# Optimization experiments

Measured on AMD Instinct MI355X. Metric: run time of the kernel, lower is better.

## Reference

```python
import jax, jax.numpy as jnp
import numpy as np

B, S, D, H = 2, 2048, 1024, 16
HD = D // H  # head_dim = 64


def setup_inputs() -> dict:
    key = jax.random.key(0)
    ks = jax.random.split(key, 7)
    scale = 0.02
    return {
        "q": jax.random.normal(ks[0], (B, S, D), dtype=jnp.float32),
        "k": jax.random.normal(ks[1], (B, S, D), dtype=jnp.float32),
        "v": jax.random.normal(ks[2], (B, S, D), dtype=jnp.float32),
        "Wq": jax.random.normal(ks[3], (D, D), dtype=jnp.float32) * scale,
        "Wk": jax.random.normal(ks[4], (D, D), dtype=jnp.float32) * scale,
        "Wv": jax.random.normal(ks[5], (D, D), dtype=jnp.float32) * scale,
        "Wo": jax.random.normal(ks[6], (D, D), dtype=jnp.float32) * scale,
    }


def reference(q, k, v, Wq, Wk, Wv, Wo):
    # bias-free linear projections (torch Linear: y = x @ W.T)
    qh = (q @ Wq.T).reshape(B, S, H, HD).transpose(0, 2, 1, 3)  # b h t d
    kh = (k @ Wk.T).reshape(B, S, H, HD).transpose(0, 2, 1, 3)
    vh = (v @ Wv.T).reshape(B, S, H, HD).transpose(0, 2, 1, 3)

    scores = jnp.einsum("bhqd,bhkd->bhqk", qh, kh) / jnp.sqrt(jnp.float32(HD))
    # max_subtract: NOTE faithful to source - max taken BEFORE causal masking
    scores = scores - jnp.max(scores, axis=-1, keepdims=True)
    # causal mask (strict upper triangle -> -inf)
    causal_mask = jnp.triu(jnp.ones((S, S), dtype=bool), k=1)
    scores = jnp.where(causal_mask, -jnp.inf, scores)
    num = jnp.exp(scores)
    den = jnp.sum(num, axis=-1, keepdims=True) + 1.0  # quiet softmax (+1 denominator)
    attn = num / den

    out = jnp.einsum("bhqk,bhkd->bhqd", attn, vh)
    out = out.transpose(0, 2, 1, 3).reshape(B, S, D)  # b t (h d)
    return out @ Wo.T
```

## Files before the change

### kernel.cpp

```cpp
#include <hip/hip_runtime.h>
#include <hip/hip_bf16.h>

#define B_  2
#define S_  2048
#define D_  1024
#define H_  16
#define HD_ 64

typedef __attribute__((ext_vector_type(4))) short s16x4;
typedef __attribute__((ext_vector_type(8))) short s16x8;
typedef __attribute__((ext_vector_type(4))) float f32x4;
typedef __attribute__((ext_vector_type(8))) __bf16 bf16x8;

__device__ __forceinline__ unsigned short f2bf(float x) {
  union { float f; unsigned int u; } un; un.f = x;
  unsigned int r = un.u + 0x7fffu + ((un.u >> 16) & 1u);
  return (unsigned short)(r >> 16);
}

__device__ __forceinline__ f32x4 fz4() { f32x4 z = {0.f, 0.f, 0.f, 0.f}; return z; }

__device__ __forceinline__ f32x4 mfma32(s16x8 a, s16x8 b, f32x4 c) {
  return __builtin_amdgcn_mfma_f32_16x16x32_bf16(
      __builtin_bit_cast(bf16x8, a), __builtin_bit_cast(bf16x8, b), c, 0, 0, 0);
}

__device__ __forceinline__ void gload16(void* lds_base, const void* gsrc) {
  __builtin_amdgcn_global_load_lds(
      (const __attribute__((address_space(1))) unsigned int*)gsrc,
      (__attribute__((address_space(3))) unsigned int*)lds_base, 16, 0, 0);
}

__global__ __launch_bounds__(256) void cvt_all(const float4* __restrict__ q,
                                               const float4* __restrict__ k,
                                               const float4* __restrict__ v,
                                               const float4* __restrict__ wq,
                                               const float4* __restrict__ wk,
                                               const float4* __restrict__ wv,
                                               const float4* __restrict__ wo,
                                               uint2* __restrict__ oq, uint2* __restrict__ ok,
                                               uint2* __restrict__ ov, uint2* __restrict__ owq,
                                               uint2* __restrict__ owk, uint2* __restrict__ owv,
                                               uint2* __restrict__ owo) {
  int i = blockIdx.x * 256 + threadIdx.x;
  int st = gridDim.x * 256;
  for (; i < 4194304; i += st) {
    const float4* s; uint2* d; int off;
    if (i < 3145728) {
      int t = i >> 20; off = i & 1048575;
      s = (t == 0) ? q : (t == 1 ? k : v);
      d = (t == 0) ? oq : (t == 1 ? ok : ov);
    } else {
      int j = i - 3145728;
      int t = j >> 18; off = j & 262143;
      s = (t == 0) ? wq : (t == 1 ? wk : (t == 2 ? wv : wo));
      d = (t == 0) ? owq : (t == 1 ? owk : (t == 2 ? owv : owo));
    }
    float4 x = s[off];
    uint2 o;
    o.x = (unsigned)f2bf(x.x) | ((unsigned)f2bf(x.y) << 16);
    o.y = (unsigned)f2bf(x.z) | ((unsigned)f2bf(x.w) << 16);
    d[off] = o;
  }
}

template<int BM, int MODE, int NG>
__global__ __launch_bounds__(256) void gemm_bt(
    const unsigned short* __restrict__ A0, const unsigned short* __restrict__ A1,
    const unsigned short* __restrict__ A2,
    const unsigned short* __restrict__ W0, const unsigned short* __restrict__ W1,
    const unsigned short* __restrict__ W2,
    unsigned short* __restrict__ ob0, unsigned short* __restrict__ ob1,
    unsigned short* __restrict__ ob2, float* __restrict__ of) {
  __shared__ unsigned short As[2][BM * 32];
  __shared__ unsigned short Bs[2][128 * 32];
  const int tid  = threadIdx.x;
  const int lane = tid & 63;
  const int w    = tid >> 6;
  const int l15  = lane & 15, g = lane >> 4;

  int m0, n0;
  const unsigned short *A, *W;
  unsigned short* obf;
  float scale = 1.0f;
  if (NG == 3) {
    int swz = ((int)blockIdx.x & 7) * 96 + ((int)blockIdx.x >> 3);
    int p  = swz >> 5;
    int gi = p >> 3;
    n0 = (p & 7) * 128;
    m0 = (swz & 31) * 128;
    A   = gi == 0 ? A0 : (gi == 1 ? A1 : A2);
    W   = gi == 0 ? W0 : (gi == 1 ? W1 : W2);
    obf = gi == 0 ? ob0 : (gi == 1 ? ob1 : ob2);
    scale = (gi == 0) ? 0.125f : 1.0f;
  } else {
    int swz = ((int)blockIdx.x & 7) * 64 + ((int)blockIdx.x >> 3);
    m0 = (swz & 63) * BM;
    n0 = (swz >> 6) * 128;
    A = A0; W = W0; obf = ob0;
  }

  constexpr int MI  = (BM == 128) ? 4 : 2;
  const int wr = (w >> 1) * (MI * 16);
  const int wc = (w & 1) * 64;

  f32x4 acc[MI][4];
  #pragma unroll
  for (int i = 0; i < MI; i++)
    #pragma unroll
    for (int j = 0; j < 4; j++) acc[i][j] = fz4();

  const int srow = w * 16 + (lane >> 2);
  const int scol = ((lane & 3) ^ ((lane >> 2) & 3)) * 8;

  #define STAGE(buf, k0)                                                          \
    {                                                                             \
      _Pragma("unroll")                                                           \
      for (int i = 0; i < BM / 64; i++)                                           \
        gload16(&As[buf][(i * 64 + w * 16) * 32],                                 \
                &A[(size_t)(m0 + i * 64 + srow) * D_ + (k0) + scol]);             \
      _Pragma("unroll")                                                           \
      for (int i = 0; i < 2; i++)                                                 \
        gload16(&Bs[buf][(i * 64 + w * 16) * 32],                                 \
                &W[(size_t)(n0 + i * 64 + srow) * D_ + (k0) + scol]);             \
    }

  STAGE(0, 0);
  __syncthreads();
  int buf = 0;
  for (int t = 0; t < 32; ++t) {
    if (t < 31) STAGE(buf ^ 1, (t + 1) * 32);
    s16x8 af[MI], bfr[4];
    #pragma unroll
    for (int mi = 0; mi < MI; mi++)
      af[mi] = *(const s16x8*)&As[buf][(wr + mi * 16 + l15) * 32 + ((g ^ (l15 & 3)) * 8)];
    #pragma unroll
    for (int ni = 0; ni < 4; ni++)
      bfr[ni] = *(const s16x8*)&Bs[buf][(wc + ni * 16 + l15) * 32 + ((g ^ (l15 & 3)) * 8)];
    __builtin_amdgcn_s_setprio(1);
    #pragma unroll
    for (int mi = 0; mi < MI; mi++)
      #pragma unroll
      for (int ni = 0; ni < 4; ni++)
        acc[mi][ni] = mfma32(af[mi], bfr[ni], acc[mi][ni]);
    __builtin_amdgcn_s_setprio(0);
    __syncthreads();
    buf ^= 1;
  }
  #undef STAGE

  #pragma unroll
  for (int mi = 0; mi < MI; mi++)
    #pragma unroll
    for (int ni = 0; ni < 4; ni++)
      #pragma unroll
      for (int j = 0; j < 4; j++) {
        int r = m0 + wr + mi * 16 + 4 * g + j;
        int c = n0 + wc + ni * 16 + l15;
        float v = acc[mi][ni][j] * scale;
        if (MODE == 0) {
          int b = r >> 11, s = r & (S_ - 1), h = c >> 6, hd = c & 63;
          obf[(((size_t)(b * H_ + h)) * S_ + s) * HD_ + hd] = f2bf(v);
        } else {
          of[(size_t)r * D_ + c] = v;
        }
      }
}

__global__ __launch_bounds__(256) void attn_kernel(const unsigned short* __restrict__ Qh,
                                                   const unsigned short* __restrict__ Kh,
                                                   const unsigned short* __restrict__ Vh,
                                                   unsigned short* __restrict__ AO) {
  __shared__ unsigned short Ks[2][64 * 64];
  __shared__ unsigned short Vt[2][64 * 76];
  const int tid  = threadIdx.x;
  const int lane = tid & 63;
  const int w    = tid >> 6;
  const int l15  = lane & 15, g = lane >> 4;

  int swz = (blockIdx.x & 7) * 128 + (blockIdx.x >> 3);
  const int qt = swz & 31;
  const int bh = swz >> 5;
  const int q0 = qt * 64;
  const unsigned short* Qb = Qh + (size_t)bh * S_ * HD_;
  const unsigned short* Kb = Kh + (size_t)bh * S_ * HD_;
  const unsigned short* Vb = Vh + (size_t)bh * S_ * HD_;

  const int qrow = q0 + w * 16 + l15;
  s16x8 qf[2];
  #pragma unroll
  for (int kk = 0; kk < 2; kk++)
    qf[kk] = *(const s16x8*)&Qb[(size_t)qrow * HD_ + kk * 32 + 8 * g];

  float m = -INFINITY, l = 0.f;
  f32x4 outa[4];
  #pragma unroll
  for (int d = 0; d < 4; d++) outa[d] = fz4();

  const int srow = w * 8 + (lane >> 3);
  const int scol = ((lane & 7) ^ ((lane >> 3) & 7)) * 8;
  const int vkey = tid & 63;

  #define STAGE_K(kblk, b)                                                        \
    {                                                                             \
      _Pragma("unroll")                                                           \
      for (int i = 0; i < 2; i++)                                                 \
        gload16(&Ks[b][(i * 256 + w * 64) * 8],                                   \
                &Kb[(size_t)((kblk) * 64 + i * 32 + srow) * HD_ + scol]);         \
    }
  #define LOAD_V(kblk, vr)                                                        \
    {                                                                             \
      _Pragma("unroll")                                                           \
      for (int r = 0; r < 2; r++)                                                 \
        vr[r] = *(const uint4*)&Vb[(size_t)((kblk) * 64 + vkey) * HD_ + (w + r * 4) * 8]; \
    }
  #define WRITE_V(b, vr)                                                          \
    {                                                                             \
      _Pragma("unroll")                                                           \
      for (int r = 0; r < 2; r++) {                                               \
        int hd0 = (w + r * 4) * 8;                                                \
        unsigned int u[4] = {vr[r].x, vr[r].y, vr[r].z, vr[r].w};                 \
        _Pragma("unroll")                                                         \
        for (int c2 = 0; c2 < 4; c2++) {                                          \
          Vt[b][(hd0 + 2 * c2    ) * 76 + vkey] = (unsigned short)(u[c2] & 0xffffu); \
          Vt[b][(hd0 + 2 * c2 + 1) * 76 + vkey] = (unsigned short)(u[c2] >> 16);  \
        }                                                                         \
      }                                                                           \
    }

  {
    STAGE_K(0, 0);
    uint4 vr0[2];
    LOAD_V(0, vr0);
    WRITE_V(0, vr0);
    __syncthreads();
  }

  for (int t = 0; t < 32; ++t) {
    const int cur = t & 1, o = cur ^ 1;
    const int k0 = t * 64;
    if (t < 31) STAGE_K(t + 1, o);
    uint4 vr[2];
    const bool vnext = (t < 31) && (t + 1 <= qt);
    if (vnext) LOAD_V(t + 1, vr);

    f32x4 sf[4];
    #pragma unroll
    for (int kt = 0; kt < 4; kt++) sf[kt] = fz4();
    __builtin_amdgcn_s_setprio(1);
    #pragma unroll
    for (int kt = 0; kt < 4; kt++)
      #pragma unroll
      for (int kk = 0; kk < 2; kk++) {
        s16x8 kf = *(const s16x8*)&Ks[cur][(kt * 16 + l15) * 64 + (((kk * 4 + g) ^ (l15 & 7)) * 8)];
        sf[kt] = mfma32(kf, qf[kk], sf[kt]);
      }
    __builtin_amdgcn_s_setprio(0);

    float bm = -INFINITY;
    #pragma unroll
    for (int kt = 0; kt < 4; kt++)
      #pragma unroll
      for (int j = 0; j < 4; j++) bm = fmaxf(bm, sf[kt][j]);
    bm = fmaxf(bm, __shfl_xor(bm, 16));
    bm = fmaxf(bm, __shfl_xor(bm, 32));
    if (__any(bm > m)) {
      float mn  = fmaxf(m, bm);
      float fsc = __expf(m - mn);
      m = mn;
      l *= fsc;
      float frow[4];
      #pragma unroll
      for (int j = 0; j < 4; j++) frow[j] = __shfl(fsc, 4 * g + j);
      #pragma unroll
      for (int d = 0; d < 4; d++)
        #pragma unroll
        for (int j = 0; j < 4; j++) outa[d][j] *= frow[j];
    }

    if (t <= qt) {
      s16x8 pfs[2];
      float rs = 0.f;
      #pragma unroll
      for (int kt2 = 0; kt2 < 2; kt2++) {
        #pragma unroll
        for (int j = 0; j < 4; j++) {
          int keyg = k0 + kt2 * 32 + 4 * g + j;
          float e = (keyg <= qrow) ? __expf(sf[2 * kt2][j] - m) : 0.f;
          rs += e;
          pfs[kt2][j] = (short)f2bf(e);
          float e2 = (keyg + 16 <= qrow) ? __expf(sf[2 * kt2 + 1][j] - m) : 0.f;
          rs += e2;
          pfs[kt2][4 + j] = (short)f2bf(e2);
        }
      }
      rs += __shfl_xor(rs, 16);
      rs += __shfl_xor(rs, 32);
      l += rs;
      __builtin_amdgcn_s_setprio(1);
      #pragma unroll
      for (int d = 0; d < 4; d++)
        #pragma unroll
        for (int kt2 = 0; kt2 < 2; kt2++) {
          s16x4 vlo = *(const s16x4*)&Vt[cur][(d * 16 + l15) * 76 + kt2 * 32 + 4 * g];
          s16x4 vhi = *(const s16x4*)&Vt[cur][(d * 16 + l15) * 76 + kt2 * 32 + 16 + 4 * g];
          s16x8 vv = {vlo[0], vlo[1], vlo[2], vlo[3], vhi[0], vhi[1], vhi[2], vhi[3]};
          outa[d] = mfma32(pfs[kt2], vv, outa[d]);
        }
      __builtin_amdgcn_s_setprio(0);
    }

    if (vnext) WRITE_V(o, vr);
    __syncthreads();
  }
  #undef STAGE_K
  #undef LOAD_V
  #undef WRITE_V

  float inv = 1.f / (l + 1.f);
  float invr[4];
  #pragma unroll
  for (int j = 0; j < 4; j++) invr[j] = __shfl(inv, 4 * g + j);
  const int b = bh >> 4, h = bh & 15;
  #pragma unroll
  for (int d = 0; d < 4; d++)
    #pragma unroll
    for (int j = 0; j < 4; j++) {
      int row = q0 + w * 16 + 4 * g + j;
      int col = h * 64 + d * 16 + l15;
      AO[(size_t)(b * S_ + row) * D_ + col] = f2bf(outa[d][j] * invr[j]);
    }
}

extern "C" void kernel_launch(void* const* d_in, const int* in_sizes, int n_in,
                              void* d_out, int out_size, void* d_ws, size_t ws_size,
                              hipStream_t stream) {
  const float* q  = (const float*)d_in[0];
  const float* k  = (const float*)d_in[1];
  const float* v  = (const float*)d_in[2];
  const float* Wq = (const float*)d_in[3];
  const float* Wk = (const float*)d_in[4];
  const float* Wv = (const float*)d_in[5];
  const float* Wo = (const float*)d_in[6];

  unsigned short* ws  = (unsigned short*)d_ws;
  unsigned short* qb  = ws;
  unsigned short* kb  = qb  + 4194304;
  unsigned short* vb  = kb  + 4194304;
  unsigned short* Wqb = vb  + 4194304;
  unsigned short* Wkb = Wqb + 1048576;
  unsigned short* Wvb = Wkb + 1048576;
  unsigned short* Wob = Wvb + 1048576;
  unsigned short* Qh  = Wob + 1048576;
  unsigned short* Kh  = Qh  + 4194304;
  unsigned short* Vh  = Kh  + 4194304;
  unsigned short* AO  = Vh  + 4194304;

  cvt_all<<<2048, 256, 0, stream>>>((const float4*)q, (const float4*)k, (const float4*)v,
                                    (const float4*)Wq, (const float4*)Wk, (const float4*)Wv,
                                    (const float4*)Wo,
                                    (uint2*)qb, (uint2*)kb, (uint2*)vb, (uint2*)Wqb,
                                    (uint2*)Wkb, (uint2*)Wvb, (uint2*)Wob);

  gemm_bt<128, 0, 3><<<768, 256, 0, stream>>>(qb, kb, vb, Wqb, Wkb, Wvb,
                                              Qh, Kh, Vh, nullptr);

  attn_kernel<<<1024, 256, 0, stream>>>(Qh, Kh, Vh, AO);

  gemm_bt<64, 1, 1><<<512, 256, 0, stream>>>(AO, nullptr, nullptr, Wob, nullptr, nullptr,
                                             nullptr, nullptr, nullptr, (float*)d_out);
}
```

Measured before the change: 252.7 us.

## Pair complementary causal query tiles per 512-thread block sharing K/V staging

Each block now runs 8 waves covering two query tiles (pr and 31-pr), so every block does a balanced amount of causal work and the staged K/V tiles are shared by both tiles. The PV MFMA operands are swapped so each lane owns a whole query row, which removes the row-scale shuffles and allows packed 8-byte output stores. The mask check is now done only on the diagonal tile. The cost is more threads per block with larger launch bounds and a barrier shared by both groups, and the group with the shorter tile sits idle through the later iterations.

```diff
diff --git a/kernel.cpp b/kernel.cpp
--- a/kernel.cpp
+++ b/kernel.cpp
@@ -167,7 +167,7 @@
       }
 }
 
-__global__ __launch_bounds__(256) void attn_kernel(const unsigned short* __restrict__ Qh,
+__global__ __launch_bounds__(512) void attn_kernel(const unsigned short* __restrict__ Qh,
                                                    const unsigned short* __restrict__ Kh,
                                                    const unsigned short* __restrict__ Vh,
                                                    unsigned short* __restrict__ AO) {
@@ -176,17 +176,22 @@
   const int tid  = threadIdx.x;
   const int lane = tid & 63;
   const int w    = tid >> 6;
+  const int wq   = w & 3;
+  const int grp  = w >> 2;
   const int l15  = lane & 15, g = lane >> 4;
 
-  int swz = (blockIdx.x & 7) * 128 + (blockIdx.x >> 3);
-  const int qt = swz & 31;
-  const int bh = swz >> 5;
-  const int q0 = qt * 64;
+  int swz = ((int)blockIdx.x & 7) * 64 + ((int)blockIdx.x >> 3);
+  const int bh = swz >> 4;
+  const int pr = swz & 15;
+  const int qtA = pr, qtB = 31 - pr;
+  const int myqt  = grp ? qtB : qtA;
+  const int qtMax = qtB;
+  const int q0 = myqt * 64;
   const unsigned short* Qb = Qh + (size_t)bh * S_ * HD_;
   const unsigned short* Kb = Kh + (size_t)bh * S_ * HD_;
   const unsigned short* Vb = Vh + (size_t)bh * S_ * HD_;
 
-  const int qrow = q0 + w * 16 + l15;
+  const int qrow = q0 + wq * 16 + l15;
   s16x8 qf[2];
   #pragma unroll
   for (int kk = 0; kk < 2; kk++)
@@ -197,51 +202,40 @@
   #pragma unroll
   for (int d = 0; d < 4; d++) outa[d] = fz4();
 
-  const int srow = w * 8 + (lane >> 3);
+  const int srow_l = lane >> 3;
   const int scol = ((lane & 7) ^ ((lane >> 3) & 7)) * 8;
   const int vkey = tid & 63;
+  const int vhd0 = (tid >> 6) * 8;
 
   #define STAGE_K(kblk, b)                                                        \
-    {                                                                             \
-      _Pragma("unroll")                                                           \
-      for (int i = 0; i < 2; i++)                                                 \
-        gload16(&Ks[b][(i * 256 + w * 64) * 8],                                   \
-                &Kb[(size_t)((kblk) * 64 + i * 32 + srow) * HD_ + scol]);         \
-    }
+    gload16(&Ks[b][(w * 8) * 64],                                                 \
+            &Kb[(size_t)((kblk) * 64 + w * 8 + srow_l) * HD_ + scol]);
   #define LOAD_V(kblk, vr)                                                        \
-    {                                                                             \
-      _Pragma("unroll")                                                           \
-      for (int r = 0; r < 2; r++)                                                 \
-        vr[r] = *(const uint4*)&Vb[(size_t)((kblk) * 64 + vkey) * HD_ + (w + r * 4) * 8]; \
-    }
+    vr = *(const uint4*)&Vb[(size_t)((kblk) * 64 + vkey) * HD_ + vhd0];
   #define WRITE_V(b, vr)                                                          \
     {                                                                             \
+      unsigned int u[4] = {vr.x, vr.y, vr.z, vr.w};                               \
       _Pragma("unroll")                                                           \
-      for (int r = 0; r < 2; r++) {                                               \
-        int hd0 = (w + r * 4) * 8;                                                \
-        unsigned int u[4] = {vr[r].x, vr[r].y, vr[r].z, vr[r].w};                 \
-        _Pragma("unroll")                                                         \
-        for (int c2 = 0; c2 < 4; c2++) {                                          \
-          Vt[b][(hd0 + 2 * c2    ) * 76 + vkey] = (unsigned short)(u[c2] & 0xffffu); \
-          Vt[b][(hd0 + 2 * c2 + 1) * 76 + vkey] = (unsigned short)(u[c2] >> 16);  \
-        }                                                                         \
+      for (int c2 = 0; c2 < 4; c2++) {                                            \
+        Vt[b][(vhd0 + 2 * c2    ) * 76 + vkey] = (unsigned short)(u[c2] & 0xffffu); \
+        Vt[b][(vhd0 + 2 * c2 + 1) * 76 + vkey] = (unsigned short)(u[c2] >> 16);   \
       }                                                                           \
     }
 
   {
     STAGE_K(0, 0);
-    uint4 vr0[2];
+    uint4 vr0;
     LOAD_V(0, vr0);
     WRITE_V(0, vr0);
     __syncthreads();
   }
 
   for (int t = 0; t < 32; ++t) {
-    const int cur = t & 1, o = cur ^ 1;
+    const int cur = t & 1, nxt = cur ^ 1;
     const int k0 = t * 64;
-    if (t < 31) STAGE_K(t + 1, o);
-    uint4 vr[2];
-    const bool vnext = (t < 31) && (t + 1 <= qt);
+    if (t < 31) STAGE_K(t + 1, nxt);
+    uint4 vr;
+    const bool vnext = (t < 31) && (t + 1 <= qtMax);
     if (vnext) LOAD_V(t + 1, vr);
 
     f32x4 sf[4];
@@ -269,30 +263,40 @@
       float fsc = __expf(m - mn);
       m = mn;
       l *= fsc;
-      float frow[4];
-      #pragma unroll
-      for (int j = 0; j < 4; j++) frow[j] = __shfl(fsc, 4 * g + j);
       #pragma unroll
       for (int d = 0; d < 4; d++)
         #pragma unroll
-        for (int j = 0; j < 4; j++) outa[d][j] *= frow[j];
-    }
-
-    if (t <= qt) {
+        for (int j = 0; j < 4; j++) outa[d][j] *= fsc;
+    }
+
+    if (t <= myqt) {
       s16x8 pfs[2];
       float rs = 0.f;
-      #pragma unroll
-      for (int kt2 = 0; kt2 < 2; kt2++) {
+      if (t == myqt) {
         #pragma unroll
-        for (int j = 0; j < 4; j++) {
-          int keyg = k0 + kt2 * 32 + 4 * g + j;
-          float e = (keyg <= qrow) ? __expf(sf[2 * kt2][j] - m) : 0.f;
-          rs += e;
-          pfs[kt2][j] = (short)f2bf(e);
-          float e2 = (keyg + 16 <= qrow) ? __expf(sf[2 * kt2 + 1][j] - m) : 0.f;
-          rs += e2;
-          pfs[kt2][4 + j] = (short)f2bf(e2);
-        }
+        for (int kt2 = 0; kt2 < 2; kt2++)
+          #pragma unroll
+          for (int j = 0; j < 4; j++) {
+            int keyg = k0 + kt2 * 32 + 4 * g + j;
+            float e = (keyg <= qrow) ? __expf(sf[2 * kt2][j] - m) : 0.f;
+            rs += e;
+            pfs[kt2][j] = (short)f2bf(e);
+            float e2 = (keyg + 16 <= qrow) ? __expf(sf[2 * kt2 + 1][j] - m) : 0.f;
+            rs += e2;
+            pfs[kt2][4 + j] = (short)f2bf(e2);
+          }
+      } else {
+        #pragma unroll
+        for (int kt2 = 0; kt2 < 2; kt2++)
+          #pragma unroll
+          for (int j = 0; j < 4; j++) {
+            float e = __expf(sf[2 * kt2][j] - m);
+            rs += e;
+            pfs[kt2][j] = (short)f2bf(e);
+            float e2 = __expf(sf[2 * kt2 + 1][j] - m);
+            rs += e2;
+            pfs[kt2][4 + j] = (short)f2bf(e2);
+          }
       }
       rs += __shfl_xor(rs, 16);
       rs += __shfl_xor(rs, 32);
@@ -305,31 +309,27 @@
           s16x4 vlo = *(const s16x4*)&Vt[cur][(d * 16 + l15) * 76 + kt2 * 32 + 4 * g];
           s16x4 vhi = *(const s16x4*)&Vt[cur][(d * 16 + l15) * 76 + kt2 * 32 + 16 + 4 * g];
           s16x8 vv = {vlo[0], vlo[1], vlo[2], vlo[3], vhi[0], vhi[1], vhi[2], vhi[3]};
-          outa[d] = mfma32(pfs[kt2], vv, outa[d]);
+          outa[d] = mfma32(vv, pfs[kt2], outa[d]);
         }
       __builtin_amdgcn_s_setprio(0);
     }
 
-    if (vnext) WRITE_V(o, vr);
+    if (vnext) WRITE_V(nxt, vr);
     __syncthreads();
   }
   #undef STAGE_K
   #undef LOAD_V
   #undef WRITE_V
 
-  float inv = 1.f / (l + 1.f);
-  float invr[4];
-  #pragma unroll
-  for (int j = 0; j < 4; j++) invr[j] = __shfl(inv, 4 * g + j);
+  const float inv = 1.f / (l + 1.f);
   const int b = bh >> 4, h = bh & 15;
   #pragma unroll
-  for (int d = 0; d < 4; d++)
-    #pragma unroll
-    for (int j = 0; j < 4; j++) {
-      int row = q0 + w * 16 + 4 * g + j;
-      int col = h * 64 + d * 16 + l15;
-      AO[(size_t)(b * S_ + row) * D_ + col] = f2bf(outa[d][j] * invr[j]);
-    }
+  for (int d = 0; d < 4; d++) {
+    uint2 o;
+    o.x = (unsigned)f2bf(outa[d][0] * inv) | ((unsigned)f2bf(outa[d][1] * inv) << 16);
+    o.y = (unsigned)f2bf(outa[d][2] * inv) | ((unsigned)f2bf(outa[d][3] * inv) << 16);
+    *(uint2*)&AO[(size_t)(b * S_ + qrow) * D_ + h * 64 + d * 16 + 4 * g] = o;
+  }
 }
 
 extern "C" void kernel_launch(void* const* d_in, const int* in_sizes, int n_in,
@@ -365,7 +365,7 @@
   gemm_bt<128, 0, 3><<<768, 256, 0, stream>>>(qb, kb, vb, Wqb, Wkb, Wvb,
                                               Qh, Kh, Vh, nullptr);
 
-  attn_kernel<<<1024, 256, 0, stream>>>(Qh, Kh, Vh, AO);
+  attn_kernel<<<512, 512, 0, stream>>>(Qh, Kh, Vh, AO);
 
   gemm_bt<64, 1, 1><<<512, 256, 0, stream>>>(AO, nullptr, nullptr, Wob, nullptr, nullptr,
                                              nullptr, nullptr, nullptr, (float*)d_out);
```

After: 223.9 us. 1.13x faster.
